# Kernel tuning notes

Measured on AMD Instinct MI355X. Metric: run time of the kernel, lower is better.

The kernel has to match this reference:

```python
import jax, jax.numpy as jnp
import numpy as np

NEG = -1000000000.0  # mask value used by the original module

def setup_inputs() -> dict:
    key = jax.random.key(0)
    kq, kk, kv, kl = jax.random.split(key, 4)
    B, Lq, Lk, D, Dv = 16, 2048, 2048, 64, 64
    q = jax.random.normal(kq, (B, Lq, D), dtype=jnp.float32)
    k = jax.random.normal(kk, (B, Lk, D), dtype=jnp.float32)
    v = jax.random.normal(kv, (B, Lk, Dv), dtype=jnp.float32)
    valid_len = jax.random.randint(kl, (B, Lq), 0, Lk, dtype=jnp.int32)
    return {"q": q, "k": k, "v": v, "valid_len": valid_len}

def reference(q, k, v, valid_len):
    # scores: [B, Lq, Lk]  (NOTE: original module does NOT scale by sqrt(d))
    scores = jnp.einsum('bqd,bkd->bqk', q, k)
    Lk = k.shape[1]
    # per-(batch,query) valid length masking over the key dimension
    mask = jnp.arange(Lk, dtype=valid_len.dtype)[None, None, :] < valid_len[:, :, None]
    scores = jnp.where(mask, scores, NEG)
    attn = jax.nn.softmax(scores, axis=-1)
    # dropout p=0.0 -> identity
    return jnp.einsum('bqk,bkv->bqv', attn, v)
```

## Files before the change

kernel.cpp:

```cpp
#include <hip/hip_runtime.h>

typedef _Float16 f16;
typedef __attribute__((ext_vector_type(8))) _Float16 f16x8;
typedef __attribute__((ext_vector_type(4))) _Float16 f16x4;
typedef __attribute__((ext_vector_type(4))) float f32x4;

#define NB 16
#define LSEQ 2048
#define DIM 64
#define KVB 64
#define QT 64
#define NT (LSEQ / KVB)
#define PITCH 72
#define LOG2E 1.44269504088896340736f

__device__ inline f16x4 pkcvt(const f32x4 x) {
    auto a = __builtin_amdgcn_cvt_pkrtz(x[0], x[1]);
    auto b = __builtin_amdgcn_cvt_pkrtz(x[2], x[3]);
    f16x4 t; t[0]=(f16)a[0]; t[1]=(f16)a[1]; t[2]=(f16)b[0]; t[3]=(f16)b[1];
    return t;
}

__global__ void build_perm(const int* __restrict__ vlg, int* __restrict__ perm) {
    const int b = blockIdx.x, tid = threadIdx.x;
    __shared__ int hist[NT + 1];
    __shared__ int base[NT + 1];
    if (tid <= NT) hist[tid] = 0;
    __syncthreads();
    for (int q = tid; q < LSEQ; q += 256) {
        int vl = vlg[b * LSEQ + q];
        int t = (vl == 0) ? NT : ((vl + KVB - 1) >> 6);
        atomicAdd(&hist[t], 1);
    }
    __syncthreads();
    if (tid == 0) {
        int acc = 0;
        for (int t = NT; t >= 0; --t) { base[t] = acc; acc += hist[t]; }
    }
    __syncthreads();
    for (int q = tid; q < LSEQ; q += 256) {
        int vl = vlg[b * LSEQ + q];
        int t = (vl == 0) ? NT : ((vl + KVB - 1) >> 6);
        int pos = atomicAdd(&base[t], 1);
        perm[b * LSEQ + pos] = q;
    }
}

__global__ __launch_bounds__(256, 3) void attn_fwd(
    const float* __restrict__ qg, const float* __restrict__ kg,
    const float* __restrict__ vg, const int* __restrict__ vlg,
    float* __restrict__ outg, const int* __restrict__ perm,
    float* __restrict__ opart, float* __restrict__ mlg,
    int sorted, int S)
{
    __shared__ alignas(16) f16 kld[2][KVB * PITCH];
    __shared__ alignas(16) f16 vtld[2][DIM * PITCH];
    __shared__ alignas(16) f16 pld[4 * 16 * PITCH];
    __shared__ int wmax[4];

    const int tid  = threadIdx.x;
    const int wid  = tid >> 6;
    const int lane = tid & 63;
    const int r    = lane & 15;
    const int hi   = lane >> 4;

    const int bid = blockIdx.x;
    const int nbs = NB * S;
    const int qt  = bid / nbs;
    const int rem = bid - qt * nbs;
    const int b   = rem / S;
    const int s   = rem - b * S;
    const int qw  = qt * QT + wid * 16;

    const int kb  = tid & 15;
    const int dvb = tid >> 4;

    const int qidx = sorted ? perm[b * LSEQ + qw + r] : (qw + r);
    const int vl   = vlg[b * LSEQ + qidx];

    int maxt;
    if (sorted) {
        int tq = (vl == 0) ? NT : ((vl + KVB - 1) >> 6);
        tq = max(tq, __shfl_xor(tq, 1));
        tq = max(tq, __shfl_xor(tq, 2));
        tq = max(tq, __shfl_xor(tq, 4));
        tq = max(tq, __shfl_xor(tq, 8));
        if (lane == 0) wmax[wid] = tq;
        __syncthreads();
        maxt = max(max(wmax[0], wmax[1]), max(wmax[2], wmax[3]));
    } else {
        maxt = NT;
    }

    int vmin = vl;
    vmin = min(vmin, __shfl_xor(vmin, 1));
    vmin = min(vmin, __shfl_xor(vmin, 2));
    vmin = min(vmin, __shfl_xor(vmin, 4));
    vmin = min(vmin, __shfl_xor(vmin, 8));

    f16x8 qf[2];
    const float* qrow = qg + ((size_t)(b * LSEQ + qidx)) * DIM;
#pragma unroll
    for (int ks = 0; ks < 2; ++ks) {
        f32x4 x = *(const f32x4*)(qrow + ks * 32 + hi * 8);
        f32x4 y = *(const f32x4*)(qrow + ks * 32 + hi * 8 + 4);
        f32x4 xs = {x[0]*LOG2E, x[1]*LOG2E, x[2]*LOG2E, x[3]*LOG2E};
        f32x4 ys = {y[0]*LOG2E, y[1]*LOG2E, y[2]*LOG2E, y[3]*LOG2E};
        f16x4 lo = pkcvt(xs), hi4 = pkcvt(ys);
        f16x8 t;
        t[0]=lo[0]; t[1]=lo[1]; t[2]=lo[2]; t[3]=lo[3];
        t[4]=hi4[0]; t[5]=hi4[1]; t[6]=hi4[2]; t[7]=hi4[3];
        qf[ks] = t;
    }

    float m_run = -INFINITY;
    float l_run = 0.0f;
    f32x4 o[4];
#pragma unroll
    for (int dt = 0; dt < 4; ++dt) o[dt] = f32x4{0.f, 0.f, 0.f, 0.f};

    f16* pw = pld + wid * (16 * PITCH);
    const float* kbase = kg + ((size_t)b * LSEQ) * DIM;
    const float* vbase = vg + ((size_t)b * LSEQ) * DIM;

    f32x4 kst[4], vst[4];

    if (s < maxt) {
        const int kv0 = s * KVB;
#pragma unroll
        for (int it = 0; it < 4; ++it) {
            int cc = tid + it * 256;
            kst[it] = *(const f32x4*)(kbase + (size_t)(kv0 + (cc >> 4)) * DIM + (cc & 15) * 4);
        }
#pragma unroll
        for (int i = 0; i < 4; ++i)
            vst[i] = *(const f32x4*)(vbase + (size_t)(kv0 + kb * 4 + i) * DIM + dvb * 4);
#pragma unroll
        for (int it = 0; it < 4; ++it) {
            int cc = tid + it * 256;
            *(f16x4*)(&kld[0][(cc >> 4) * PITCH + (cc & 15) * 4]) = pkcvt(kst[it]);
        }
#pragma unroll
        for (int j = 0; j < 4; ++j) {
            f32x4 col = {vst[0][j], vst[1][j], vst[2][j], vst[3][j]};
            *(f16x4*)(&vtld[0][(dvb * 4 + j) * PITCH + kb * 4]) = pkcvt(col);
        }
    }

    int c = 0;
    for (int tt = s; tt < maxt; tt += S) {
        __syncthreads();

        const int nt_ = tt + S;
        if (nt_ < maxt) {
            const int kv0n = nt_ * KVB;
#pragma unroll
            for (int it = 0; it < 4; ++it) {
                int cc = tid + it * 256;
                kst[it] = *(const f32x4*)(kbase + (size_t)(kv0n + (cc >> 4)) * DIM + (cc & 15) * 4);
            }
#pragma unroll
            for (int i = 0; i < 4; ++i)
                vst[i] = *(const f32x4*)(vbase + (size_t)(kv0n + kb * 4 + i) * DIM + dvb * 4);
        }

        f32x4 st[4];
        __builtin_amdgcn_s_setprio(1);
#pragma unroll
        for (int kt = 0; kt < 4; ++kt) {
            f32x4 acc = f32x4{0.f, 0.f, 0.f, 0.f};
#pragma unroll
            for (int ks = 0; ks < 2; ++ks) {
                f16x8 kf = *(const f16x8*)(&kld[c][(kt * 16 + r) * PITCH + ks * 32 + hi * 8]);
                acc = __builtin_amdgcn_mfma_f32_16x16x32_f16(kf, qf[ks], acc, 0, 0, 0);
            }
            st[kt] = acc;
        }
        __builtin_amdgcn_s_setprio(0);

        const int kv0 = tt * KVB;
        float tmax = -INFINITY;
        if (kv0 + KVB > vmin) {
#pragma unroll
            for (int kt = 0; kt < 4; ++kt)
#pragma unroll
                for (int g = 0; g < 4; ++g) {
                    int key = kv0 + kt * 16 + hi * 4 + g;
                    float sc = (key < vl) ? st[kt][g] : -1e9f;
                    st[kt][g] = sc;
                    tmax = fmaxf(tmax, sc);
                }
        } else {
#pragma unroll
            for (int kt = 0; kt < 4; ++kt)
#pragma unroll
                for (int g = 0; g < 4; ++g)
                    tmax = fmaxf(tmax, st[kt][g]);
        }
        tmax = fmaxf(tmax, __shfl_xor(tmax, 16));
        tmax = fmaxf(tmax, __shfl_xor(tmax, 32));
        float m_new = fmaxf(m_run, tmax);
        float scale = exp2f(m_run - m_new);
        float tsum = 0.0f;
#pragma unroll
        for (int kt = 0; kt < 4; ++kt) {
            f16x4 pv;
#pragma unroll
            for (int g = 0; g < 4; ++g) {
                float p = exp2f(st[kt][g] - m_new);
                tsum += p;
                pv[g] = (f16)p;
            }
            *(f16x4*)(pw + r * PITCH + kt * 16 + hi * 4) = pv;
        }
        tsum += __shfl_xor(tsum, 16);
        tsum += __shfl_xor(tsum, 32);
        l_run = l_run * scale + tsum;
        m_run = m_new;

#pragma unroll
        for (int g = 0; g < 4; ++g) {
            float sc = __shfl(scale, hi * 4 + g);
#pragma unroll
            for (int dt = 0; dt < 4; ++dt) o[dt][g] *= sc;
        }

        __builtin_amdgcn_s_setprio(1);
#pragma unroll
        for (int ks = 0; ks < 2; ++ks) {
            f16x8 pa = *(const f16x8*)(pw + r * PITCH + ks * 32 + hi * 8);
#pragma unroll
            for (int dt = 0; dt < 4; ++dt) {
                f16x8 vf = *(const f16x8*)(&vtld[c][(dt * 16 + r) * PITCH + ks * 32 + hi * 8]);
                o[dt] = __builtin_amdgcn_mfma_f32_16x16x32_f16(pa, vf, o[dt], 0, 0, 0);
            }
        }
        __builtin_amdgcn_s_setprio(0);

        if (nt_ < maxt) {
#pragma unroll
            for (int it = 0; it < 4; ++it) {
                int cc = tid + it * 256;
                *(f16x4*)(&kld[c ^ 1][(cc >> 4) * PITCH + (cc & 15) * 4]) = pkcvt(kst[it]);
            }
#pragma unroll
            for (int j = 0; j < 4; ++j) {
                f32x4 col = {vst[0][j], vst[1][j], vst[2][j], vst[3][j]};
                *(f16x4*)(&vtld[c ^ 1][(dvb * 4 + j) * PITCH + kb * 4]) = pkcvt(col);
            }
        }
        c ^= 1;
    }

    if (S == 1) {
        float inv = 1.0f / l_run;
#pragma unroll
        for (int g = 0; g < 4; ++g) {
            float iv = __shfl(inv, hi * 4 + g);
            int   qo = __shfl(qidx, hi * 4 + g);
            float* ob = outg + ((size_t)(b * LSEQ + qo)) * DIM;
#pragma unroll
            for (int dt = 0; dt < 4; ++dt)
                ob[dt * 16 + r] = o[dt][g] * iv;
        }
    } else {
        float* obase = opart + ((size_t)s * NB * LSEQ + (size_t)b * LSEQ) * DIM;
#pragma unroll
        for (int g = 0; g < 4; ++g) {
            int qo = __shfl(qidx, hi * 4 + g);
            float* ob = obase + (size_t)qo * DIM;
#pragma unroll
            for (int dt = 0; dt < 4; ++dt)
                ob[dt * 16 + r] = o[dt][g];
        }
        if (hi == 0) {
            size_t mi = ((size_t)s * NB * LSEQ + (size_t)b * LSEQ + qidx) * 2;
            mlg[mi]     = m_run;
            mlg[mi + 1] = l_run;
        }
    }
}

__global__ void merge_k(const float* __restrict__ opart, const float* __restrict__ mlg,
                        float* __restrict__ outg, int S)
{
    const int gt = blockIdx.x * 256 + threadIdx.x;
    const size_t base = (size_t)gt * 4;
    const size_t qg = base >> 6;
    float M = -INFINITY;
    for (int s = 0; s < S; ++s)
        M = fmaxf(M, mlg[((size_t)s * NB * LSEQ + qg) * 2]);
    float den = 0.f;
    f32x4 acc = {0.f, 0.f, 0.f, 0.f};
    for (int s = 0; s < S; ++s) {
        size_t mi = ((size_t)s * NB * LSEQ + qg) * 2;
        float w = exp2f(mlg[mi] - M);
        den += w * mlg[mi + 1];
        f32x4 ov = *(const f32x4*)(opart + (size_t)s * NB * LSEQ * DIM + base);
        acc[0] += w * ov[0]; acc[1] += w * ov[1];
        acc[2] += w * ov[2]; acc[3] += w * ov[3];
    }
    float inv = 1.0f / den;
    f32x4 res = {acc[0]*inv, acc[1]*inv, acc[2]*inv, acc[3]*inv};
    *(f32x4*)(outg + base) = res;
}

extern "C" void kernel_launch(void* const* d_in, const int* in_sizes, int n_in,
                              void* d_out, int out_size, void* d_ws, size_t ws_size,
                              hipStream_t stream) {
    const float* q  = (const float*)d_in[0];
    const float* k  = (const float*)d_in[1];
    const float* v  = (const float*)d_in[2];
    const int*   vl = (const int*)d_in[3];
    float* out = (float*)d_out;

    const size_t perm_b = (size_t)NB * LSEQ * sizeof(int);
    auto need = [&](int S) {
        return perm_b + (size_t)S * NB * LSEQ * DIM * sizeof(float)
                      + (size_t)S * NB * LSEQ * 2 * sizeof(float);
    };
    int S, sorted;
    if      (d_ws && ws_size >= need(4)) { S = 4; sorted = 1; }
    else if (d_ws && ws_size >= need(2)) { S = 2; sorted = 1; }
    else if (d_ws && ws_size >= perm_b)  { S = 1; sorted = 1; }
    else                                 { S = 1; sorted = 0; }

    int*   perm  = (int*)d_ws;
    float* opart = (float*)((char*)d_ws + perm_b);
    float* mlg   = opart + (size_t)S * NB * LSEQ * DIM;

    if (sorted) build_perm<<<NB, 256, 0, stream>>>(vl, perm);

    attn_fwd<<<dim3(NB * (LSEQ / QT) * S), dim3(256), 0, stream>>>(
        q, k, v, vl, out, perm, opart, mlg, sorted, S);

    if (S > 1) {
        const int mthreads = NB * LSEQ * DIM / 4;
        merge_k<<<dim3(mthreads / 256), dim3(256), 0, stream>>>(opart, mlg, out, S);
    }
}
```

Measured before the change: 54.15 us.

## Pre-convert K/V to swizzled fp16 and stage tiles via direct global-to-LDS loads

Adds a kvprep kernel that converts K and V to fp16 once, writing K row-major and V transposed, both with an XOR swizzle. The attention kernel then fills its double-buffered LDS tiles with global_load_lds instead of loading fp32 into registers, converting and storing. This removes the redundant per-block conversion and halves the K/V bytes read. The online softmax now rescales only when a new max exceeds the running max by a threshold, and the row sum is reduced across lanes once at the end rather than every tile. Split partial outputs are stored in fp16. The cost is an extra kernel launch, a larger workspace, and slightly lower precision in the partial outputs.

```diff
diff --git a/kernel.cpp b/kernel.cpp
--- a/kernel.cpp
+++ b/kernel.cpp
@@ -19,6 +19,12 @@
     auto b = __builtin_amdgcn_cvt_pkrtz(x[2], x[3]);
     f16x4 t; t[0]=(f16)a[0]; t[1]=(f16)a[1]; t[2]=(f16)b[0]; t[3]=(f16)b[1];
     return t;
+}
+
+__device__ inline void gload16(const void* g, void* l) {
+    __builtin_amdgcn_global_load_lds(
+        (const __attribute__((address_space(1))) unsigned int*)g,
+        (__attribute__((address_space(3))) unsigned int*)l, 16, 0, 0);
 }
 
 __global__ void build_perm(const int* __restrict__ vlg, int* __restrict__ perm) {
@@ -46,15 +52,47 @@
     }
 }
 
+__global__ __launch_bounds__(256) void kvprep(
+    const float* __restrict__ kg, const float* __restrict__ vg,
+    f16* __restrict__ k16, f16* __restrict__ v16)
+{
+    const int bt = blockIdx.x;
+    const int b = bt >> 5, t = bt & 31;
+    const int tid = threadIdx.x;
+    const float* kb_ = kg + ((size_t)b * LSEQ + t * KVB) * DIM;
+    const float* vb_ = vg + ((size_t)b * LSEQ + t * KVB) * DIM;
+    f16* kd = k16 + (size_t)bt * (KVB * DIM);
+    f16* vd = v16 + (size_t)bt * (KVB * DIM);
+#pragma unroll
+    for (int it = 0; it < 4; ++it) {
+        int cc = tid + it * 256;
+        int row = cc >> 4, c4 = (cc & 15) * 4;
+        f32x4 x = *(const f32x4*)(kb_ + row * DIM + c4);
+        *(f16x4*)(kd + row * 64 + (c4 ^ ((row & 7) * 8))) = pkcvt(x);
+    }
+    {
+        int kb4 = tid & 15, dvb = tid >> 4;
+        f32x4 rr[4];
+#pragma unroll
+        for (int i = 0; i < 4; ++i)
+            rr[i] = *(const f32x4*)(vb_ + (size_t)(kb4 * 4 + i) * DIM + dvb * 4);
+#pragma unroll
+        for (int j = 0; j < 4; ++j) {
+            int dv = dvb * 4 + j;
+            f32x4 col = {rr[0][j], rr[1][j], rr[2][j], rr[3][j]};
+            *(f16x4*)(vd + dv * 64 + ((kb4 * 4) ^ ((dv & 7) * 8))) = pkcvt(col);
+        }
+    }
+}
+
 __global__ __launch_bounds__(256, 3) void attn_fwd(
-    const float* __restrict__ qg, const float* __restrict__ kg,
-    const float* __restrict__ vg, const int* __restrict__ vlg,
+    const float* __restrict__ qg, const int* __restrict__ vlg,
+    const f16* __restrict__ k16, const f16* __restrict__ v16,
     float* __restrict__ outg, const int* __restrict__ perm,
-    float* __restrict__ opart, float* __restrict__ mlg,
-    int sorted, int S)
+    f16* __restrict__ opart, float* __restrict__ mlg, int S)
 {
-    __shared__ alignas(16) f16 kld[2][KVB * PITCH];
-    __shared__ alignas(16) f16 vtld[2][DIM * PITCH];
+    __shared__ alignas(16) f16 kbuf[2][KVB * 64];
+    __shared__ alignas(16) f16 vbuf[2][DIM * 64];
     __shared__ alignas(16) f16 pld[4 * 16 * PITCH];
     __shared__ int wmax[4];
 
@@ -72,25 +110,17 @@
     const int s   = rem - b * S;
     const int qw  = qt * QT + wid * 16;
 
-    const int kb  = tid & 15;
-    const int dvb = tid >> 4;
-
-    const int qidx = sorted ? perm[b * LSEQ + qw + r] : (qw + r);
+    const int qidx = perm[b * LSEQ + qw + r];
     const int vl   = vlg[b * LSEQ + qidx];
 
-    int maxt;
-    if (sorted) {
-        int tq = (vl == 0) ? NT : ((vl + KVB - 1) >> 6);
-        tq = max(tq, __shfl_xor(tq, 1));
-        tq = max(tq, __shfl_xor(tq, 2));
-        tq = max(tq, __shfl_xor(tq, 4));
-        tq = max(tq, __shfl_xor(tq, 8));
-        if (lane == 0) wmax[wid] = tq;
-        __syncthreads();
-        maxt = max(max(wmax[0], wmax[1]), max(wmax[2], wmax[3]));
-    } else {
-        maxt = NT;
-    }
+    int tq = (vl == 0) ? NT : ((vl + KVB - 1) >> 6);
+    tq = max(tq, __shfl_xor(tq, 1));
+    tq = max(tq, __shfl_xor(tq, 2));
+    tq = max(tq, __shfl_xor(tq, 4));
+    tq = max(tq, __shfl_xor(tq, 8));
+    if (lane == 0) wmax[wid] = tq;
+    __syncthreads();
+    const int maxt = max(max(wmax[0], wmax[1]), max(wmax[2], wmax[3]));
 
     int vmin = vl;
     vmin = min(vmin, __shfl_xor(vmin, 1));
@@ -106,10 +136,10 @@
         f32x4 y = *(const f32x4*)(qrow + ks * 32 + hi * 8 + 4);
         f32x4 xs = {x[0]*LOG2E, x[1]*LOG2E, x[2]*LOG2E, x[3]*LOG2E};
         f32x4 ys = {y[0]*LOG2E, y[1]*LOG2E, y[2]*LOG2E, y[3]*LOG2E};
-        f16x4 lo = pkcvt(xs), hi4 = pkcvt(ys);
+        f16x4 lo = pkcvt(xs), hh = pkcvt(ys);
         f16x8 t;
         t[0]=lo[0]; t[1]=lo[1]; t[2]=lo[2]; t[3]=lo[3];
-        t[4]=hi4[0]; t[5]=hi4[1]; t[6]=hi4[2]; t[7]=hi4[3];
+        t[4]=hh[0]; t[5]=hh[1]; t[6]=hh[2]; t[7]=hh[3];
         qf[ks] = t;
     }
 
@@ -120,49 +150,26 @@
     for (int dt = 0; dt < 4; ++dt) o[dt] = f32x4{0.f, 0.f, 0.f, 0.f};
 
     f16* pw = pld + wid * (16 * PITCH);
-    const float* kbase = kg + ((size_t)b * LSEQ) * DIM;
-    const float* vbase = vg + ((size_t)b * LSEQ) * DIM;
-
-    f32x4 kst[4], vst[4];
-
-    if (s < maxt) {
-        const int kv0 = s * KVB;
-#pragma unroll
-        for (int it = 0; it < 4; ++it) {
-            int cc = tid + it * 256;
-            kst[it] = *(const f32x4*)(kbase + (size_t)(kv0 + (cc >> 4)) * DIM + (cc & 15) * 4);
-        }
-#pragma unroll
-        for (int i = 0; i < 4; ++i)
-            vst[i] = *(const f32x4*)(vbase + (size_t)(kv0 + kb * 4 + i) * DIM + dvb * 4);
-#pragma unroll
-        for (int it = 0; it < 4; ++it) {
-            int cc = tid + it * 256;
-            *(f16x4*)(&kld[0][(cc >> 4) * PITCH + (cc & 15) * 4]) = pkcvt(kst[it]);
-        }
-#pragma unroll
-        for (int j = 0; j < 4; ++j) {
-            f32x4 col = {vst[0][j], vst[1][j], vst[2][j], vst[3][j]};
-            *(f16x4*)(&vtld[0][(dvb * 4 + j) * PITCH + kb * 4]) = pkcvt(col);
-        }
-    }
-
+    const f16* kt_base = k16 + (size_t)b * (NT * KVB * DIM);
+    const f16* vt_base = v16 + (size_t)b * (NT * KVB * DIM);
+    const int swz = (r & 7) * 8;
+
+    auto stage = [&](int bi, int t) {
+        const char* ks = (const char*)(kt_base + (size_t)t * 4096);
+        const char* vs = (const char*)(vt_base + (size_t)t * 4096);
+        char* kd = (char*)&kbuf[bi][0];
+        char* vd = (char*)&vbuf[bi][0];
+        gload16(ks + tid * 16,        kd + tid * 16);
+        gload16(ks + 4096 + tid * 16, kd + 4096 + tid * 16);
+        gload16(vs + tid * 16,        vd + tid * 16);
+        gload16(vs + 4096 + tid * 16, vd + 4096 + tid * 16);
+    };
+
+    if (s < maxt) stage(0, s);
     int c = 0;
     for (int tt = s; tt < maxt; tt += S) {
         __syncthreads();
-
-        const int nt_ = tt + S;
-        if (nt_ < maxt) {
-            const int kv0n = nt_ * KVB;
-#pragma unroll
-            for (int it = 0; it < 4; ++it) {
-                int cc = tid + it * 256;
-                kst[it] = *(const f32x4*)(kbase + (size_t)(kv0n + (cc >> 4)) * DIM + (cc & 15) * 4);
-            }
-#pragma unroll
-            for (int i = 0; i < 4; ++i)
-                vst[i] = *(const f32x4*)(vbase + (size_t)(kv0n + kb * 4 + i) * DIM + dvb * 4);
-        }
+        if (tt + S < maxt) stage(c ^ 1, tt + S);
 
         f32x4 st[4];
         __builtin_amdgcn_s_setprio(1);
@@ -171,7 +178,7 @@
             f32x4 acc = f32x4{0.f, 0.f, 0.f, 0.f};
 #pragma unroll
             for (int ks = 0; ks < 2; ++ks) {
-                f16x8 kf = *(const f16x8*)(&kld[c][(kt * 16 + r) * PITCH + ks * 32 + hi * 8]);
+                f16x8 kf = *(const f16x8*)(&kbuf[c][(kt * 16 + r) * 64 + ((ks * 32 + hi * 8) ^ swz)]);
                 acc = __builtin_amdgcn_mfma_f32_16x16x32_f16(kf, qf[ks], acc, 0, 0, 0);
             }
             st[kt] = acc;
@@ -179,51 +186,52 @@
         __builtin_amdgcn_s_setprio(0);
 
         const int kv0 = tt * KVB;
-        float tmax = -INFINITY;
+        float lanemax = -INFINITY;
         if (kv0 + KVB > vmin) {
 #pragma unroll
             for (int kt = 0; kt < 4; ++kt)
 #pragma unroll
                 for (int g = 0; g < 4; ++g) {
                     int key = kv0 + kt * 16 + hi * 4 + g;
-                    float sc = (key < vl) ? st[kt][g] : -1e9f;
-                    st[kt][g] = sc;
-                    tmax = fmaxf(tmax, sc);
+                    float sv = (key < vl) ? st[kt][g] : -1e9f;
+                    st[kt][g] = sv;
+                    lanemax = fmaxf(lanemax, sv);
                 }
         } else {
 #pragma unroll
             for (int kt = 0; kt < 4; ++kt)
 #pragma unroll
                 for (int g = 0; g < 4; ++g)
-                    tmax = fmaxf(tmax, st[kt][g]);
-        }
-        tmax = fmaxf(tmax, __shfl_xor(tmax, 16));
-        tmax = fmaxf(tmax, __shfl_xor(tmax, 32));
-        float m_new = fmaxf(m_run, tmax);
-        float scale = exp2f(m_run - m_new);
-        float tsum = 0.0f;
+                    lanemax = fmaxf(lanemax, st[kt][g]);
+        }
+
+        if (__any(lanemax > m_run + 8.0f)) {
+            float tmax = lanemax;
+            tmax = fmaxf(tmax, __shfl_xor(tmax, 16));
+            tmax = fmaxf(tmax, __shfl_xor(tmax, 32));
+            float m_new = fmaxf(m_run, tmax);
+            float scale = exp2f(m_run - m_new);
+            l_run *= scale;
+            m_run = m_new;
+#pragma unroll
+            for (int g = 0; g < 4; ++g) {
+                float sc = __shfl(scale, hi * 4 + g);
+#pragma unroll
+                for (int dt = 0; dt < 4; ++dt) o[dt][g] *= sc;
+            }
+        }
+
 #pragma unroll
         for (int kt = 0; kt < 4; ++kt) {
             f16x4 pv;
 #pragma unroll
             for (int g = 0; g < 4; ++g) {
-                float p = exp2f(st[kt][g] - m_new);
-                tsum += p;
+                float p = exp2f(st[kt][g] - m_run);
+                l_run += p;
                 pv[g] = (f16)p;
             }
             *(f16x4*)(pw + r * PITCH + kt * 16 + hi * 4) = pv;
         }
-        tsum += __shfl_xor(tsum, 16);
-        tsum += __shfl_xor(tsum, 32);
-        l_run = l_run * scale + tsum;
-        m_run = m_new;
-
-#pragma unroll
-        for (int g = 0; g < 4; ++g) {
-            float sc = __shfl(scale, hi * 4 + g);
-#pragma unroll
-            for (int dt = 0; dt < 4; ++dt) o[dt][g] *= sc;
-        }
 
         __builtin_amdgcn_s_setprio(1);
 #pragma unroll
@@ -231,26 +239,16 @@
             f16x8 pa = *(const f16x8*)(pw + r * PITCH + ks * 32 + hi * 8);
 #pragma unroll
             for (int dt = 0; dt < 4; ++dt) {
-                f16x8 vf = *(const f16x8*)(&vtld[c][(dt * 16 + r) * PITCH + ks * 32 + hi * 8]);
+                f16x8 vf = *(const f16x8*)(&vbuf[c][(dt * 16 + r) * 64 + ((ks * 32 + hi * 8) ^ swz)]);
                 o[dt] = __builtin_amdgcn_mfma_f32_16x16x32_f16(pa, vf, o[dt], 0, 0, 0);
             }
         }
         __builtin_amdgcn_s_setprio(0);
-
-        if (nt_ < maxt) {
-#pragma unroll
-            for (int it = 0; it < 4; ++it) {
-                int cc = tid + it * 256;
-                *(f16x4*)(&kld[c ^ 1][(cc >> 4) * PITCH + (cc & 15) * 4]) = pkcvt(kst[it]);
-            }
-#pragma unroll
-            for (int j = 0; j < 4; ++j) {
-                f32x4 col = {vst[0][j], vst[1][j], vst[2][j], vst[3][j]};
-                *(f16x4*)(&vtld[c ^ 1][(dvb * 4 + j) * PITCH + kb * 4]) = pkcvt(col);
-            }
-        }
         c ^= 1;
     }
+
+    l_run += __shfl_xor(l_run, 16);
+    l_run += __shfl_xor(l_run, 32);
 
     if (S == 1) {
         float inv = 1.0f / l_run;
@@ -264,14 +262,14 @@
                 ob[dt * 16 + r] = o[dt][g] * iv;
         }
     } else {
-        float* obase = opart + ((size_t)s * NB * LSEQ + (size_t)b * LSEQ) * DIM;
+        f16* obase = opart + ((size_t)s * NB * LSEQ + (size_t)b * LSEQ) * DIM;
 #pragma unroll
         for (int g = 0; g < 4; ++g) {
             int qo = __shfl(qidx, hi * 4 + g);
-            float* ob = obase + (size_t)qo * DIM;
+            f16* ob = obase + (size_t)qo * DIM;
 #pragma unroll
             for (int dt = 0; dt < 4; ++dt)
-                ob[dt * 16 + r] = o[dt][g];
+                ob[dt * 16 + r] = (f16)o[dt][g];
         }
         if (hi == 0) {
             size_t mi = ((size_t)s * NB * LSEQ + (size_t)b * LSEQ + qidx) * 2;
@@ -281,7 +279,7 @@
     }
 }
 
-__global__ void merge_k(const float* __restrict__ opart, const float* __restrict__ mlg,
+__global__ void merge_k(const f16* __restrict__ opart, const float* __restrict__ mlg,
                         float* __restrict__ outg, int S)
 {
     const int gt = blockIdx.x * 256 + threadIdx.x;
@@ -296,9 +294,9 @@
         size_t mi = ((size_t)s * NB * LSEQ + qg) * 2;
         float w = exp2f(mlg[mi] - M);
         den += w * mlg[mi + 1];
-        f32x4 ov = *(const f32x4*)(opart + (size_t)s * NB * LSEQ * DIM + base);
-        acc[0] += w * ov[0]; acc[1] += w * ov[1];
-        acc[2] += w * ov[2]; acc[3] += w * ov[3];
+        f16x4 ov = *(const f16x4*)(opart + (size_t)s * (NB * LSEQ * DIM) + base);
+        acc[0] += w * (float)ov[0]; acc[1] += w * (float)ov[1];
+        acc[2] += w * (float)ov[2]; acc[3] += w * (float)ov[3];
     }
     float inv = 1.0f / den;
     f32x4 res = {acc[0]*inv, acc[1]*inv, acc[2]*inv, acc[3]*inv};
@@ -315,24 +313,29 @@
     float* out = (float*)d_out;
 
     const size_t perm_b = (size_t)NB * LSEQ * sizeof(int);
+    const size_t kv_b   = (size_t)NB * LSEQ * DIM * sizeof(f16);
     auto need = [&](int S) {
-        return perm_b + (size_t)S * NB * LSEQ * DIM * sizeof(float)
-                      + (size_t)S * NB * LSEQ * 2 * sizeof(float);
+        return perm_b + 2 * kv_b
+             + (size_t)S * NB * LSEQ * 2 * sizeof(float)
+             + (size_t)S * NB * LSEQ * DIM * sizeof(f16);
     };
-    int S, sorted;
-    if      (d_ws && ws_size >= need(4)) { S = 4; sorted = 1; }
-    else if (d_ws && ws_size >= need(2)) { S = 2; sorted = 1; }
-    else if (d_ws && ws_size >= perm_b)  { S = 1; sorted = 1; }
-    else                                 { S = 1; sorted = 0; }
+    int S;
+    if      (ws_size >= need(4)) S = 4;
+    else if (ws_size >= need(2)) S = 2;
+    else                         S = 1;
 
     int*   perm  = (int*)d_ws;
-    float* opart = (float*)((char*)d_ws + perm_b);
-    float* mlg   = opart + (size_t)S * NB * LSEQ * DIM;
-
-    if (sorted) build_perm<<<NB, 256, 0, stream>>>(vl, perm);
+    f16*   k16   = (f16*)((char*)d_ws + perm_b);
+    f16*   v16   = (f16*)((char*)d_ws + perm_b + kv_b);
+    float* mlg   = (float*)((char*)d_ws + perm_b + 2 * kv_b);
+    f16*   opart = (f16*)((char*)d_ws + perm_b + 2 * kv_b
+                          + (size_t)S * NB * LSEQ * 2 * sizeof(float));
+
+    build_perm<<<NB, 256, 0, stream>>>(vl, perm);
+    kvprep<<<NB * NT, 256, 0, stream>>>(k, v, k16, v16);
 
     attn_fwd<<<dim3(NB * (LSEQ / QT) * S), dim3(256), 0, stream>>>(
-        q, k, v, vl, out, perm, opart, mlg, sorted, S);
+        q, vl, k16, v16, out, perm, opart, mlg, S);
 
     if (S > 1) {
         const int mthreads = NB * LSEQ * DIM / 4;
```

Result: faster. 51.93 us (-4.1%).
